# Optimization experiments

Hardware: AMD Instinct MI355X
Metric: run time of the kernel (lower is better)

The kernel has to match this reference:

```python
import jax, jax.numpy as jnp
import numpy as np
from jax import lax

ALPHA = 1.5
N_ITER = 100


def entmax(z, alpha=ALPHA, n_iter=N_ITER):
    # z: [B, Sq, Sk] scores. Bisection for the entmax threshold tau.
    z = (alpha - 1.0) * z.astype(jnp.float32)
    S = z.shape[-1]
    z_max = jnp.max(z, axis=-1, keepdims=True)          # [B, Sq, 1]
    tau_min = z_max - 1.0
    tau_max = z_max - np.float32(S ** (1.0 - alpha))
    inv = 1.0 / (alpha - 1.0)                            # = 2.0 for alpha=1.5

    def body(carry, _):
        tmin, tmax, _ = carry
        tau = (tmin + tmax) * 0.5
        p = jnp.maximum(z - tau, 0.0) ** inv             # [B, Sq, Sk]
        Z = jnp.sum(p, axis=-1, keepdims=True)           # [B, Sq, 1]
        tmin = jnp.where(Z >= 1.0, tau, tmin)
        tmax = jnp.where(Z < 1.0, tau, tmax)
        return (tmin, tmax, tau), None

    init = (tau_min, tau_max, (tau_min + tau_max) * 0.5)
    (tmin, tmax, tau), _ = lax.scan(jax.checkpoint(body), init, None, length=n_iter)
    # faithful to the TF code: final output uses p, Z from the LAST iteration's tau
    p = jnp.maximum(z - tau, 0.0) ** inv
    Z = jnp.sum(p, axis=-1, keepdims=True)
    return p / Z


def setup_inputs() -> dict:
    key = jax.random.key(0)
    kq, kk, kv = jax.random.split(key, 3)
    B, S, D = 8, 2048, 128
    return {
        "query": jax.random.normal(kq, (B, S, D), dtype=jnp.float32),
        "key": jax.random.normal(kk, (B, S, D), dtype=jnp.float32),
        "value": jax.random.normal(kv, (B, S, D), dtype=jnp.float32),
    }


def reference(query, key, value):
    scores = jnp.einsum("bqd,bkd->bqk", query, key)      # QK^T, no scaling (as in source)
    weights = entmax(scores, alpha=ALPHA, n_iter=N_ITER)
    return jnp.einsum("bqk,bkd->bqd", weights, value)
```

## Files before the change

### kernel.cpp

```cpp
#include <hip/hip_runtime.h>

#define BB 8
#define SS 2048
#define DD 128
#define ROWS 16
#define NW 8
#define CTW 16

typedef short bf16x8 __attribute__((ext_vector_type(8)));
typedef float f32x4 __attribute__((ext_vector_type(4)));

template <int I> struct IC { static constexpr int value = I; };
template <int I, int N, typename F>
__device__ __forceinline__ void sfor(F&& f) {
  if constexpr (I < N) { f(IC<I>{}); sfor<I + 1, N>((F&&)f); }
}

__device__ __forceinline__ short f2bf(float x) {
  return __builtin_bit_cast(short, (__bf16)x);
}
__device__ __forceinline__ float bf2f(short u) {
  return __uint_as_float(((unsigned)(unsigned short)u) << 16);
}

__device__ __forceinline__ void stage_tile(const short* g, short* l) {
#pragma unroll
  for (int s = 0; s < 4; ++s) {
    __builtin_amdgcn_global_load_lds(
        (const __attribute__((address_space(1))) void*)(g + (s << 9)),
        (__attribute__((address_space(3))) void*)(l + (s << 9)), 16, 0, 0);
  }
}

__global__ __launch_bounds__(256)
void ksplit(const float* __restrict__ K, short* __restrict__ Khi) {
  const int lin  = blockIdx.x * 256 + threadIdx.x;
  const int b    = lin >> 15;
  const int rem  = lin & 32767;
  const int ct   = rem >> 8;
  const int s    = (rem >> 6) & 3;
  const int lane = rem & 63;
  const int quad = lane >> 4, m16 = lane & 15;
  const size_t elem = (size_t)(b * SS + ct * 16 + m16) * DD + s * 32 + quad * 8;
  const float4 v0 = *(const float4*)(K + elem);
  const float4 v1 = *(const float4*)(K + elem + 4);
  const float f[8] = {v0.x, v0.y, v0.z, v0.w, v1.x, v1.y, v1.z, v1.w};
  bf16x8 h;
#pragma unroll
  for (int e = 0; e < 8; ++e) h[e] = f2bf(f[e]);
  *(bf16x8*)(Khi + (size_t)lin * 8) = h;
}

__global__ __launch_bounds__(512) __attribute__((amdgpu_waves_per_eu(4)))
void attn(const float* __restrict__ Q, const short* __restrict__ Khi,
          const float* __restrict__ K, const float* __restrict__ V,
          float* __restrict__ Out) {
  __shared__ short kring[NW][2][2048];
  __shared__ unsigned short Qs[ROWS][136];
  __shared__ float rbuf[ROWS][64];
  __shared__ int   scol[ROWS][64];
  __shared__ float exM[NW][ROWS];
  __shared__ float exZ[NW][ROWS];
  __shared__ int   rcnt[ROWS];
  __shared__ float tauB[ROWS], ZB[ROWS];
  __shared__ int   flagv;

  const int tid  = threadIdx.x;
  const int lane = tid & 63;
  const int wid  = __builtin_amdgcn_readfirstlane(tid >> 6);
  const int quad = lane >> 4, m16 = lane & 15;
  const int b    = blockIdx.x & 7;
  const int qt   = blockIdx.x >> 3;

  const float* Qb = Q + (size_t)(b * SS + qt * ROWS) * DD;
  const float* Kb = K + (size_t)b * SS * DD;
  const float* Vb = V + (size_t)b * SS * DD;
  float*       Ob = Out + (size_t)(b * SS + qt * ROWS) * DD;
  const short* KHb = Khi + (size_t)b * SS * DD;

  if (tid < ROWS) rcnt[tid] = 0;
  if (tid == ROWS) flagv = 0;

  {
    const int row = tid >> 5, d = (tid & 31) * 4;
    const float4 v = *(const float4*)&Qb[row * DD + d];
    ushort4 h;
    h.x = (unsigned short)f2bf(0.5f * v.x);
    h.y = (unsigned short)f2bf(0.5f * v.y);
    h.z = (unsigned short)f2bf(0.5f * v.z);
    h.w = (unsigned short)f2bf(0.5f * v.w);
    *(ushort4*)&Qs[row][d] = h;
  }
  __syncthreads();

  bf16x8 qh[4];
#pragma unroll
  for (int s = 0; s < 4; ++s)
    qh[s] = *(const bf16x8*)&Qs[m16][s * 32 + quad * 8];

  short* ring0 = &kring[wid][0][0];
  short* ring1 = &kring[wid][1][0];
  const short* gw = KHb + ((size_t)(wid * CTW) << 11) + lane * 8;

  stage_tile(gw + 0 * 2048, ring0);
  stage_tile(gw + 1 * 2048, ring1);

  f32x4 acc[CTW];
  sfor<0, CTW>([&](auto ic) {
    constexpr int i = ic.value;
    if constexpr (i < CTW - 1) asm volatile("s_waitcnt vmcnt(4)" ::: "memory");
    else                       asm volatile("s_waitcnt vmcnt(0)" ::: "memory");
    const short* sbl = ((i & 1) ? ring1 : ring0) + lane * 8;
    f32x4 c = {0.f, 0.f, 0.f, 0.f};
    sfor<0, 4>([&](auto sc) {
      constexpr int s = sc.value;
      const bf16x8 bh = *(const bf16x8*)(sbl + (s << 9));
      c = __builtin_amdgcn_mfma_f32_16x16x32_bf16(qh[s], bh, c, 0, 0, 0);
    });
    acc[i] = c;
    if constexpr (i + 2 < CTW) {
      asm volatile("s_waitcnt lgkmcnt(0)" ::: "memory");
      stage_tile(gw + (i + 2) * 2048, (i & 1) ? ring1 : ring0);
    }
  });

  float mx[4] = {-1e38f, -1e38f, -1e38f, -1e38f};
  sfor<0, CTW>([&](auto ic) {
#pragma unroll
    for (int j = 0; j < 4; ++j) mx[j] = fmaxf(mx[j], acc[ic.value][j]);
  });
#pragma unroll
  for (int j = 0; j < 4; ++j)
#pragma unroll
    for (int s = 1; s <= 8; s <<= 1) mx[j] = fmaxf(mx[j], __shfl_xor(mx[j], s));
  if (m16 == 0) {
#pragma unroll
    for (int j = 0; j < 4; ++j) exM[wid][4 * quad + j] = mx[j];
  }
  __syncthreads();
  float M4[4];
#pragma unroll
  for (int j = 0; j < 4; ++j) {
    float m = -1e38f;
#pragma unroll
    for (int w = 0; w < NW; ++w) m = fmaxf(m, exM[w][4 * quad + j]);
    M4[j] = m;
  }

  sfor<0, CTW>([&](auto ic) {
    constexpr int i = ic.value;
    const int col = wid * 256 + i * 16 + m16;
#pragma unroll
    for (int j = 0; j < 4; ++j) {
      const int row = 4 * quad + j;
      if (acc[i][j] > M4[j] - 1.25f) {
        const int pos = atomicAdd(&rcnt[row], 1);
        if (pos < 64) { scol[row][pos] = col; rbuf[row][pos] = acc[i][j]; }
        else atomicOr(&flagv, 1);
      }
    }
  });
  __syncthreads();

  if (flagv == 0) {

#pragma unroll
    for (int rr = 0; rr < 2; ++rr) {
      const int row = 2 * wid + rr;
      const int n = rcnt[row];
      const float2 q2 = *(const float2*)&Qb[row * DD + lane * 2];
      for (int i = 0; i < n; ++i) {
        const int c = scol[row][i];
        const float2 k2 = *(const float2*)&Kb[(size_t)c * DD + lane * 2];
        float t = fmaf(q2.x, k2.x, q2.y * k2.y);
#pragma unroll
        for (int s = 1; s <= 32; s <<= 1) t += __shfl_xor(t, s);
        if (lane == 0) rbuf[row][i] = 0.5f * t;
      }
    }

    {
      const int rr32 = lane >> 5;
      const int row  = 2 * wid + rr32;
      const int l32  = lane & 31;
      const int n = rcnt[row];
      const float a0 = (l32 < n)      ? rbuf[row][l32]      : -1e38f;
      const float a1 = (l32 + 32 < n) ? rbuf[row][l32 + 32] : -1e38f;
      float Mr = fmaxf(a0, a1);
#pragma unroll
      for (int s = 1; s <= 16; s <<= 1) Mr = fmaxf(Mr, __shfl_xor(Mr, s));
      float tmn = Mr - 1.0f, tmx = Mr - 0.022097086912079608f;
      float tau = 0.5f * (tmn + tmx), Zr = 0.f;
      for (int it = 0; it < 100; ++it) {
        tau = 0.5f * (tmn + tmx);
        const float t0 = fmaxf(a0 - tau, 0.f);
        const float t1 = fmaxf(a1 - tau, 0.f);
        float zp = fmaf(t0, t0, t1 * t1);
#pragma unroll
        for (int s = 1; s <= 16; s <<= 1) zp += __shfl_xor(zp, s);
        Zr = zp;
        const float nmn = (zp >= 1.f) ? tau : tmn;
        const float nmx = (zp >= 1.f) ? tmx : tau;
        const bool ch = (nmn != tmn) || (nmx != tmx);
        tmn = nmn; tmx = nmx;
        if (!__any(ch)) break;
      }
      if (l32 == 0) { tauB[row] = tau; ZB[row] = Zr; }
    }

#pragma unroll
    for (int rr = 0; rr < 2; ++rr) {
      const int row = 2 * wid + rr;
      const int n = rcnt[row];
      const float tau = tauB[row];
      const float iz  = 1.0f / ZB[row];
      float2 o = {0.f, 0.f};
      for (int i = 0; i < n; ++i) {
        const float rv = rbuf[row][i];
        const float tt = fmaxf(rv - tau, 0.f);
        const float pi = tt * tt * iz;
        const int   c  = scol[row][i];
        const float2 v2 = *(const float2*)&Vb[(size_t)c * DD + lane * 2];
        o.x = fmaf(pi, v2.x, o.x);
        o.y = fmaf(pi, v2.y, o.y);
      }
      *(float2*)&Ob[row * DD + lane * 2] = o;
    }
  } else {
    float tau4[4], Z4[4];
    float tmn4[4], tmx4[4];
#pragma unroll
    for (int j = 0; j < 4; ++j) {
      tmn4[j] = M4[j] - 1.0f; tmx4[j] = M4[j] - 0.022097086912079608f;
      tau4[j] = 0.5f * (tmn4[j] + tmx4[j]); Z4[j] = 0.f;
    }
    for (int it = 0; it < 100; ++it) {
      float zp[4] = {0.f, 0.f, 0.f, 0.f};
#pragma unroll
      for (int j = 0; j < 4; ++j) tau4[j] = 0.5f * (tmn4[j] + tmx4[j]);
      sfor<0, CTW>([&](auto ic) {
#pragma unroll
        for (int j = 0; j < 4; ++j) {
          const float tt = fmaxf(acc[ic.value][j] - tau4[j], 0.f);
          zp[j] = fmaf(tt, tt, zp[j]);
        }
      });
#pragma unroll
      for (int j = 0; j < 4; ++j)
#pragma unroll
        for (int s = 1; s <= 8; s <<= 1) zp[j] += __shfl_xor(zp[j], s);
      if (m16 == 0) {
#pragma unroll
        for (int j = 0; j < 4; ++j) exZ[wid][4 * quad + j] = zp[j];
      }
      __syncthreads();
      bool ch = false;
#pragma unroll
      for (int j = 0; j < 4; ++j) {
        float Zf = 0.f;
#pragma unroll
        for (int w = 0; w < NW; ++w) Zf += exZ[w][4 * quad + j];
        Z4[j] = Zf;
        const float nmn = (Zf >= 1.f) ? tau4[j] : tmn4[j];
        const float nmx = (Zf >= 1.f) ? tmx4[j] : tau4[j];
        ch = ch || (nmn != tmn4[j]) || (nmx != tmx4[j]);
        tmn4[j] = nmn; tmx4[j] = nmx;
      }
      __syncthreads();
      if (!ch) break;
    }

    float (*obuf)[DD] = (float (*)[DD])&kring[0][0][0];
    for (int i = tid; i < ROWS * DD; i += 512) ((float*)obuf)[i] = 0.f;
    __syncthreads();
    sfor<0, CTW>([&](auto ic) {
      constexpr int i = ic.value;
      const int col = wid * 256 + i * 16 + m16;
#pragma unroll
      for (int j = 0; j < 4; ++j) {
        const int row = 4 * quad + j;
        const float tt = fmaxf(acc[i][j] - tau4[j], 0.f);
        const float p = tt * tt / Z4[j];
        if (p > 0.f) {
          for (int d = 0; d < DD; ++d)
            atomicAdd(&obuf[row][d], p * Vb[(size_t)col * DD + d]);
        }
      }
    });
    __syncthreads();
    for (int i = tid; i < ROWS * DD; i += 512) {
      const int row = i >> 7, d = i & 127;
      Ob[row * DD + d] = obuf[row][d];
    }
  }
}

extern "C" void kernel_launch(void* const* d_in, const int* in_sizes, int n_in,
                              void* d_out, int out_size, void* d_ws, size_t ws_size,
                              hipStream_t stream) {
  const float* Q = (const float*)d_in[0];
  const float* K = (const float*)d_in[1];
  const float* V = (const float*)d_in[2];
  float* out = (float*)d_out;
  short* Khi = (short*)d_ws;

  hipLaunchKernelGGL(ksplit, dim3(BB * SS * DD / (256 * 8)), dim3(256), 0, stream,
                     K, Khi);
  hipLaunchKernelGGL(attn, dim3(BB * (SS / ROWS)), dim3(512), 0, stream,
                     Q, Khi, K, V, out);
}
```

Before: 137.4 us.

## Split QK tiles into two halves to halve accumulator registers, per-row overflow fallback

Rather than keeping all 16 QK^T accumulator tiles live, the kernel now computes 8 tiles, finds the row max and collects candidate columns from them, then reuses the same registers for the next 8 tiles. Each half uses its own max as the threshold. This roughly halves the accumulator register footprint, which may cut spills or raise occupancy. The block-wide overflow flag becomes a per-row flag, and overflowing rows fall back to an exact full-row fp32 recomputation done within a single wave. Candidate collection per half may admit more columns, so rows can overflow the 64-entry buffer more often, and the new fallback path is slow.

```diff
diff --git a/kernel.cpp b/kernel.cpp
--- a/kernel.cpp
+++ b/kernel.cpp
@@ -59,11 +59,11 @@
   __shared__ unsigned short Qs[ROWS][136];
   __shared__ float rbuf[ROWS][64];
   __shared__ int   scol[ROWS][64];
-  __shared__ float exM[NW][ROWS];
-  __shared__ float exZ[NW][ROWS];
+  __shared__ float exM0[NW][ROWS];
+  __shared__ float exM1[NW][ROWS];
   __shared__ int   rcnt[ROWS];
+  __shared__ int   rovf[ROWS];
   __shared__ float tauB[ROWS], ZB[ROWS];
-  __shared__ int   flagv;
 
   const int tid  = threadIdx.x;
   const int lane = tid & 63;
@@ -78,8 +78,7 @@
   float*       Ob = Out + (size_t)(b * SS + qt * ROWS) * DD;
   const short* KHb = Khi + (size_t)b * SS * DD;
 
-  if (tid < ROWS) rcnt[tid] = 0;
-  if (tid == ROWS) flagv = 0;
+  if (tid < ROWS) { rcnt[tid] = 0; rovf[tid] = 0; }
 
   {
     const int row = tid >> 5, d = (tid & 31) * 4;
@@ -105,11 +104,11 @@
   stage_tile(gw + 0 * 2048, ring0);
   stage_tile(gw + 1 * 2048, ring1);
 
-  f32x4 acc[CTW];
-  sfor<0, CTW>([&](auto ic) {
+  f32x4 acc[8];
+
+  sfor<0, 8>([&](auto ic) {
     constexpr int i = ic.value;
-    if constexpr (i < CTW - 1) asm volatile("s_waitcnt vmcnt(4)" ::: "memory");
-    else                       asm volatile("s_waitcnt vmcnt(0)" ::: "memory");
+    asm volatile("s_waitcnt vmcnt(4)" ::: "memory");
     const short* sbl = ((i & 1) ? ring1 : ring0) + lane * 8;
     f32x4 c = {0.f, 0.f, 0.f, 0.f};
     sfor<0, 4>([&](auto sc) {
@@ -118,99 +117,155 @@
       c = __builtin_amdgcn_mfma_f32_16x16x32_bf16(qh[s], bh, c, 0, 0, 0);
     });
     acc[i] = c;
-    if constexpr (i + 2 < CTW) {
+    asm volatile("s_waitcnt lgkmcnt(0)" ::: "memory");
+    stage_tile(gw + (i + 2) * 2048, (i & 1) ? ring1 : ring0);
+  });
+
+  {
+    float mx[4] = {-1e38f, -1e38f, -1e38f, -1e38f};
+    sfor<0, 8>([&](auto ic) {
+#pragma unroll
+      for (int j = 0; j < 4; ++j) mx[j] = fmaxf(mx[j], acc[ic.value][j]);
+    });
+#pragma unroll
+    for (int j = 0; j < 4; ++j)
+#pragma unroll
+      for (int s = 1; s <= 8; s <<= 1) mx[j] = fmaxf(mx[j], __shfl_xor(mx[j], s));
+    if (m16 == 0) {
+#pragma unroll
+      for (int j = 0; j < 4; ++j) exM0[wid][4 * quad + j] = mx[j];
+    }
+  }
+  __syncthreads();
+  float M0[4];
+#pragma unroll
+  for (int j = 0; j < 4; ++j) {
+    float m = -1e38f;
+#pragma unroll
+    for (int w = 0; w < NW; ++w) m = fmaxf(m, exM0[w][4 * quad + j]);
+    M0[j] = m;
+  }
+  sfor<0, 8>([&](auto ic) {
+    constexpr int i = ic.value;
+    const int col = wid * 256 + i * 16 + m16;
+#pragma unroll
+    for (int j = 0; j < 4; ++j) {
+      const int row = 4 * quad + j;
+      if (acc[i][j] > M0[j] - 1.25f) {
+        const int pos = atomicAdd(&rcnt[row], 1);
+        if (pos < 64) { scol[row][pos] = col; rbuf[row][pos] = acc[i][j]; }
+        else rovf[row] = 1;
+      }
+    }
+  });
+
+  sfor<8, 16>([&](auto ic) {
+    constexpr int i = ic.value;
+    if constexpr (i < 15) asm volatile("s_waitcnt vmcnt(4)" ::: "memory");
+    else                  asm volatile("s_waitcnt vmcnt(0)" ::: "memory");
+    const short* sbl = ((i & 1) ? ring1 : ring0) + lane * 8;
+    f32x4 c = {0.f, 0.f, 0.f, 0.f};
+    sfor<0, 4>([&](auto sc) {
+      constexpr int s = sc.value;
+      const bf16x8 bh = *(const bf16x8*)(sbl + (s << 9));
+      c = __builtin_amdgcn_mfma_f32_16x16x32_bf16(qh[s], bh, c, 0, 0, 0);
+    });
+    acc[i - 8] = c;
+    if constexpr (i + 2 < 16) {
       asm volatile("s_waitcnt lgkmcnt(0)" ::: "memory");
       stage_tile(gw + (i + 2) * 2048, (i & 1) ? ring1 : ring0);
     }
   });
 
-  float mx[4] = {-1e38f, -1e38f, -1e38f, -1e38f};
-  sfor<0, CTW>([&](auto ic) {
-#pragma unroll
-    for (int j = 0; j < 4; ++j) mx[j] = fmaxf(mx[j], acc[ic.value][j]);
-  });
-#pragma unroll
-  for (int j = 0; j < 4; ++j)
-#pragma unroll
-    for (int s = 1; s <= 8; s <<= 1) mx[j] = fmaxf(mx[j], __shfl_xor(mx[j], s));
-  if (m16 == 0) {
-#pragma unroll
-    for (int j = 0; j < 4; ++j) exM[wid][4 * quad + j] = mx[j];
+  {
+    float mx[4] = {-1e38f, -1e38f, -1e38f, -1e38f};
+    sfor<0, 8>([&](auto ic) {
+#pragma unroll
+      for (int j = 0; j < 4; ++j) mx[j] = fmaxf(mx[j], acc[ic.value][j]);
+    });
+#pragma unroll
+    for (int j = 0; j < 4; ++j)
+#pragma unroll
+      for (int s = 1; s <= 8; s <<= 1) mx[j] = fmaxf(mx[j], __shfl_xor(mx[j], s));
+    if (m16 == 0) {
+#pragma unroll
+      for (int j = 0; j < 4; ++j) exM1[wid][4 * quad + j] = mx[j];
+    }
   }
   __syncthreads();
-  float M4[4];
+  float M1[4];
 #pragma unroll
   for (int j = 0; j < 4; ++j) {
     float m = -1e38f;
 #pragma unroll
-    for (int w = 0; w < NW; ++w) m = fmaxf(m, exM[w][4 * quad + j]);
-    M4[j] = m;
-  }
-
-  sfor<0, CTW>([&](auto ic) {
+    for (int w = 0; w < NW; ++w) m = fmaxf(m, exM1[w][4 * quad + j]);
+    M1[j] = m;
+  }
+  sfor<0, 8>([&](auto ic) {
     constexpr int i = ic.value;
-    const int col = wid * 256 + i * 16 + m16;
+    const int col = wid * 256 + (i + 8) * 16 + m16;
 #pragma unroll
     for (int j = 0; j < 4; ++j) {
       const int row = 4 * quad + j;
-      if (acc[i][j] > M4[j] - 1.25f) {
+      if (acc[i][j] > M1[j] - 1.25f) {
         const int pos = atomicAdd(&rcnt[row], 1);
         if (pos < 64) { scol[row][pos] = col; rbuf[row][pos] = acc[i][j]; }
-        else atomicOr(&flagv, 1);
+        else rovf[row] = 1;
       }
     }
   });
   __syncthreads();
 
-  if (flagv == 0) {
-
-#pragma unroll
-    for (int rr = 0; rr < 2; ++rr) {
-      const int row = 2 * wid + rr;
-      const int n = rcnt[row];
-      const float2 q2 = *(const float2*)&Qb[row * DD + lane * 2];
-      for (int i = 0; i < n; ++i) {
-        const int c = scol[row][i];
-        const float2 k2 = *(const float2*)&Kb[(size_t)c * DD + lane * 2];
-        float t = fmaf(q2.x, k2.x, q2.y * k2.y);
-#pragma unroll
-        for (int s = 1; s <= 32; s <<= 1) t += __shfl_xor(t, s);
-        if (lane == 0) rbuf[row][i] = 0.5f * t;
-      }
-    }
-
-    {
-      const int rr32 = lane >> 5;
-      const int row  = 2 * wid + rr32;
-      const int l32  = lane & 31;
-      const int n = rcnt[row];
-      const float a0 = (l32 < n)      ? rbuf[row][l32]      : -1e38f;
-      const float a1 = (l32 + 32 < n) ? rbuf[row][l32 + 32] : -1e38f;
-      float Mr = fmaxf(a0, a1);
-#pragma unroll
-      for (int s = 1; s <= 16; s <<= 1) Mr = fmaxf(Mr, __shfl_xor(Mr, s));
-      float tmn = Mr - 1.0f, tmx = Mr - 0.022097086912079608f;
-      float tau = 0.5f * (tmn + tmx), Zr = 0.f;
-      for (int it = 0; it < 100; ++it) {
-        tau = 0.5f * (tmn + tmx);
-        const float t0 = fmaxf(a0 - tau, 0.f);
-        const float t1 = fmaxf(a1 - tau, 0.f);
-        float zp = fmaf(t0, t0, t1 * t1);
-#pragma unroll
-        for (int s = 1; s <= 16; s <<= 1) zp += __shfl_xor(zp, s);
-        Zr = zp;
-        const float nmn = (zp >= 1.f) ? tau : tmn;
-        const float nmx = (zp >= 1.f) ? tmx : tau;
-        const bool ch = (nmn != tmn) || (nmx != tmx);
-        tmn = nmn; tmx = nmx;
-        if (!__any(ch)) break;
-      }
-      if (l32 == 0) { tauB[row] = tau; ZB[row] = Zr; }
-    }
-
-#pragma unroll
-    for (int rr = 0; rr < 2; ++rr) {
-      const int row = 2 * wid + rr;
+
+#pragma unroll
+  for (int rr = 0; rr < 2; ++rr) {
+    const int row = 2 * wid + rr;
+    if (rovf[row]) continue;
+    const int n = rcnt[row];
+    const float2 q2 = *(const float2*)&Qb[row * DD + lane * 2];
+    for (int i = 0; i < n; ++i) {
+      const int c = scol[row][i];
+      const float2 k2 = *(const float2*)&Kb[(size_t)c * DD + lane * 2];
+      float t = fmaf(q2.x, k2.x, q2.y * k2.y);
+#pragma unroll
+      for (int s = 1; s <= 32; s <<= 1) t += __shfl_xor(t, s);
+      if (lane == 0) rbuf[row][i] = 0.5f * t;
+    }
+  }
+
+  {
+    const int rr32 = lane >> 5;
+    const int row  = 2 * wid + rr32;
+    const int l32  = lane & 31;
+    const int n = rcnt[row] < 64 ? rcnt[row] : 64;
+    const float a0 = (l32 < n)      ? rbuf[row][l32]      : -1e38f;
+    const float a1 = (l32 + 32 < n) ? rbuf[row][l32 + 32] : -1e38f;
+    float Mr = fmaxf(a0, a1);
+#pragma unroll
+    for (int s = 1; s <= 16; s <<= 1) Mr = fmaxf(Mr, __shfl_xor(Mr, s));
+    float tmn = Mr - 1.0f, tmx = Mr - 0.022097086912079608f;
+    float tau = 0.5f * (tmn + tmx), Zr = 0.f;
+    for (int it = 0; it < 100; ++it) {
+      tau = 0.5f * (tmn + tmx);
+      const float t0 = fmaxf(a0 - tau, 0.f);
+      const float t1 = fmaxf(a1 - tau, 0.f);
+      float zp = fmaf(t0, t0, t1 * t1);
+#pragma unroll
+      for (int s = 1; s <= 16; s <<= 1) zp += __shfl_xor(zp, s);
+      Zr = zp;
+      const float nmn = (zp >= 1.f) ? tau : tmn;
+      const float nmx = (zp >= 1.f) ? tmx : tau;
+      const bool ch = (nmn != tmn) || (nmx != tmx);
+      tmn = nmn; tmx = nmx;
+      if (!__any(ch)) break;
+    }
+    if (l32 == 0) { tauB[row] = tau; ZB[row] = Zr; }
+  }
+
+#pragma unroll
+  for (int rr = 0; rr < 2; ++rr) {
+    const int row = 2 * wid + rr;
+    if (!rovf[row]) {
       const int n = rcnt[row];
       const float tau = tauB[row];
       const float iz  = 1.0f / ZB[row];
@@ -225,72 +280,54 @@
         o.y = fmaf(pi, v2.y, o.y);
       }
       *(float2*)&Ob[row * DD + lane * 2] = o;
-    }
-  } else {
-    float tau4[4], Z4[4];
-    float tmn4[4], tmx4[4];
-#pragma unroll
-    for (int j = 0; j < 4; ++j) {
-      tmn4[j] = M4[j] - 1.0f; tmx4[j] = M4[j] - 0.022097086912079608f;
-      tau4[j] = 0.5f * (tmn4[j] + tmx4[j]); Z4[j] = 0.f;
-    }
-    for (int it = 0; it < 100; ++it) {
-      float zp[4] = {0.f, 0.f, 0.f, 0.f};
-#pragma unroll
-      for (int j = 0; j < 4; ++j) tau4[j] = 0.5f * (tmn4[j] + tmx4[j]);
-      sfor<0, CTW>([&](auto ic) {
-#pragma unroll
-        for (int j = 0; j < 4; ++j) {
-          const float tt = fmaxf(acc[ic.value][j] - tau4[j], 0.f);
-          zp[j] = fmaf(tt, tt, zp[j]);
+    } else {
+      float* zr = (float*)&kring[wid][0][0];
+      for (int c0 = 0; c0 < 32; ++c0) {
+        const int c = c0 * 64 + lane;
+        const float* kp = &Kb[(size_t)c * DD];
+        float t = 0.f;
+        for (int d = 0; d < DD; d += 4) {
+          const float4 qv = *(const float4*)&Qb[row * DD + d];
+          const float4 kv = *(const float4*)&kp[d];
+          t = fmaf(qv.x, kv.x, t); t = fmaf(qv.y, kv.y, t);
+          t = fmaf(qv.z, kv.z, t); t = fmaf(qv.w, kv.w, t);
         }
-      });
-#pragma unroll
-      for (int j = 0; j < 4; ++j)
-#pragma unroll
-        for (int s = 1; s <= 8; s <<= 1) zp[j] += __shfl_xor(zp[j], s);
-      if (m16 == 0) {
-#pragma unroll
-        for (int j = 0; j < 4; ++j) exZ[wid][4 * quad + j] = zp[j];
-      }
-      __syncthreads();
-      bool ch = false;
-#pragma unroll
-      for (int j = 0; j < 4; ++j) {
-        float Zf = 0.f;
-#pragma unroll
-        for (int w = 0; w < NW; ++w) Zf += exZ[w][4 * quad + j];
-        Z4[j] = Zf;
-        const float nmn = (Zf >= 1.f) ? tau4[j] : tmn4[j];
-        const float nmx = (Zf >= 1.f) ? tmx4[j] : tau4[j];
-        ch = ch || (nmn != tmn4[j]) || (nmx != tmx4[j]);
-        tmn4[j] = nmn; tmx4[j] = nmx;
-      }
-      __syncthreads();
-      if (!ch) break;
-    }
-
-    float (*obuf)[DD] = (float (*)[DD])&kring[0][0][0];
-    for (int i = tid; i < ROWS * DD; i += 512) ((float*)obuf)[i] = 0.f;
-    __syncthreads();
-    sfor<0, CTW>([&](auto ic) {
-      constexpr int i = ic.value;
-      const int col = wid * 256 + i * 16 + m16;
-#pragma unroll
-      for (int j = 0; j < 4; ++j) {
-        const int row = 4 * quad + j;
-        const float tt = fmaxf(acc[i][j] - tau4[j], 0.f);
-        const float p = tt * tt / Z4[j];
-        if (p > 0.f) {
-          for (int d = 0; d < DD; ++d)
-            atomicAdd(&obuf[row][d], p * Vb[(size_t)col * DD + d]);
+        zr[c] = 0.5f * t;
+      }
+      float Mr = -1e38f;
+      for (int c0 = 0; c0 < 32; ++c0) Mr = fmaxf(Mr, zr[c0 * 64 + lane]);
+#pragma unroll
+      for (int s = 1; s <= 32; s <<= 1) Mr = fmaxf(Mr, __shfl_xor(Mr, s));
+      float tmn = Mr - 1.0f, tmx = Mr - 0.022097086912079608f;
+      float tau = 0.5f * (tmn + tmx), Zr = 0.f;
+      for (int it = 0; it < 100; ++it) {
+        tau = 0.5f * (tmn + tmx);
+        float zp = 0.f;
+        for (int c0 = 0; c0 < 32; ++c0) {
+          const float tt = fmaxf(zr[c0 * 64 + lane] - tau, 0.f);
+          zp = fmaf(tt, tt, zp);
         }
-      }
-    });
-    __syncthreads();
-    for (int i = tid; i < ROWS * DD; i += 512) {
-      const int row = i >> 7, d = i & 127;
-      Ob[row * DD + d] = obuf[row][d];
+#pragma unroll
+        for (int s = 1; s <= 32; s <<= 1) zp += __shfl_xor(zp, s);
+        Zr = zp;
+        const float nmn = (zp >= 1.f) ? tau : tmn;
+        const float nmx = (zp >= 1.f) ? tmx : tau;
+        const bool ch = (nmn != tmn) || (nmx != tmx);
+        tmn = nmn; tmx = nmx;
+        if (!__any(ch)) break;
+      }
+      const float iz = 1.0f / Zr;
+      float2 o = {0.f, 0.f};
+      for (int c = 0; c < SS; ++c) {
+        const float tt = fmaxf(zr[c] - tau, 0.f);
+        if (tt > 0.f) {
+          const float pi = tt * tt * iz;
+          const float2 v2 = *(const float2*)&Vb[(size_t)c * DD + lane * 2];
+          o.x = fmaf(pi, v2.x, o.x);
+          o.y = fmaf(pi, v2.y, o.y);
+        }
+      }
+      *(float2*)&Ob[row * DD + lane * 2] = o;
     }
   }
 }
```

After: 142.3 us. 3.5% more time.
